# Performance work log

Hardware: AMD Instinct MI355X
Metric: run time of the kernel (lower is better)

## Reference

```python
import jax, jax.numpy as jnp
import numpy as np

N = 100_000      # nodes
E = 1_600_000    # edges
INP = 32
OUT = 32
ATTN = 32        # attn_rel_emb_dim
NREL = 16
NBASE = 8


def setup_inputs() -> dict:
    key = jax.random.key(0)
    ks = jax.random.split(key, 12)
    s = 0.1
    h = jax.random.normal(ks[0], (N, INP), jnp.float32)
    src = jax.random.randint(ks[1], (E,), 0, N)
    dst = jax.random.randint(ks[2], (E,), 0, N)
    e_type = jax.random.randint(ks[3], (E,), 0, NREL)
    weight = jax.random.normal(ks[4], (NBASE, INP, OUT), jnp.float32) * s
    w_comp = jax.random.normal(ks[5], (NREL, NBASE), jnp.float32) * s
    self_loop_weight = jax.random.normal(ks[6], (INP, OUT), jnp.float32) * s
    bias = jax.random.normal(ks[7], (OUT,), jnp.float32) * s
    attn_emb = jax.random.normal(ks[8], (NREL, ATTN), jnp.float32) * s
    A_w = jax.random.normal(ks[9], (2 * INP + ATTN, ATTN), jnp.float32) * s
    A_b = jnp.zeros((ATTN,), jnp.float32)
    B_w = jax.random.normal(ks[10], (ATTN, 1), jnp.float32) * s
    B_b = jnp.zeros((1,), jnp.float32)
    return dict(h=h, weight=weight, w_comp=w_comp, self_loop_weight=self_loop_weight,
                bias=bias, attn_emb=attn_emb, A_w=A_w, A_b=A_b, B_w=B_w, B_b=B_b,
                src=src, dst=dst, e_type=e_type)


def reference(h, weight, w_comp, self_loop_weight, bias, attn_emb,
              A_w, A_b, B_w, B_b, src, dst, e_type):
    # basis-decomposed relation weights: [num_rels, inp, out]
    rel_w = jnp.einsum('rb,bio->rio', w_comp, weight)
    # in-degree based scale (torch.log(in_degrees + 1); scale /= scale.mean())
    in_deg = jax.ops.segment_sum(jnp.ones((E,), h.dtype), dst, num_segments=N)
    scale = jnp.log(in_deg + 1.0)
    scale = scale / jnp.mean(scale)
    # per-edge message: gather relation weight, bmm with source feature
    msg = jnp.einsum('ei,eio->eo', h[src], rel_w[e_type])          # [E, OUT]
    # attention MLP over [h_src, h_dst, rel_emb]
    feat = jnp.concatenate([h[src], h[dst], attn_emb[e_type]], axis=1)  # [E, 2*INP+ATTN]
    a = jax.nn.sigmoid(jax.nn.relu(feat @ A_w + A_b) @ B_w + B_b)  # [E, 1]
    # scatter-reduce attended messages into destination nodes
    agg = jax.ops.segment_sum(a * msg, dst, num_segments=N)        # [N, OUT]
    # self-loop term (curr_emb in the aggregator)
    curr = h @ self_loop_weight                                     # [N, OUT]
    denom = jnp.maximum(in_deg, 1.0)[:, None]  # nei_edge_count normalization
    out = curr + scale[:, None] * agg / denom + bias
    return jax.nn.relu(out)
```

## Files before the change

kernel.cpp:

```cpp
#include <hip/hip_runtime.h>
#include <hip/hip_fp16.h>
#include <cstdio>
#include <cstdint>

#define NREL 16
#define NBASE 8
#define NPB 512
#define NPLACE 256

typedef _Float16 half8 __attribute__((ext_vector_type(8)));
typedef float floatx4 __attribute__((ext_vector_type(4)));

template <int CTRL>
__device__ __forceinline__ float dpp_add_f(float x) {
    int xi = __builtin_bit_cast(int, x);
    int yi = __builtin_amdgcn_update_dpp(0, xi, CTRL, 0xF, 0xF, true);
    return x + __builtin_bit_cast(float, yi);
}

__global__ __launch_bounds__(256) void k_fused1(
        const float* __restrict__ h, const float* __restrict__ A_w,
        const float* __restrict__ slw,
        const float* __restrict__ weight, const float* __restrict__ w_comp,
        const float* __restrict__ attn_emb, const float* __restrict__ A_b,
        const int* __restrict__ dst,
        __half* __restrict__ hA1, _Float16* __restrict__ h16,
        float* __restrict__ hA2, float* __restrict__ curr,
        _Float16* __restrict__ relwB16, float* __restrict__ relA,
        int* __restrict__ histT,
        int N, int E, int nb_pre) {
    __shared__ __align__(16) float Wall[32 * 128];
    __shared__ float hbuf[32 * 33];
    __shared__ int hist[256];
    int bx = blockIdx.x;
    int t = threadIdx.x;
    if (bx < nb_pre) {
        #pragma unroll
        for (int k = 0; k < 16; ++k) {
            int idx = t + 256 * k;
            int i = idx >> 7, c = idx & 127;
            float v = 0.f;
            if (c < 32)       v = A_w[i * 32 + c];
            else if (c < 64)  v = A_w[(32 + i) * 32 + (c - 32)];
            else if (c < 96)  v = slw[i * 32 + (c - 64)];
            Wall[idx] = v;
        }
        int n0 = bx * 32;
        #pragma unroll
        for (int k = 0; k < 4; ++k) {
            int idx = t + 256 * k;
            int row = idx >> 5, col = idx & 31;
            int n = n0 + row;
            hbuf[row * 33 + col] = (n < N) ? h[n * 32 + col] : 0.f;
        }
        __syncthreads();
        int nl = t >> 3;
        int tg = t & 7;
        float4 a0 = {0,0,0,0}, a1 = {0,0,0,0}, a2 = {0,0,0,0};
        #pragma unroll 8
        for (int i = 0; i < 32; ++i) {
            float hv = hbuf[nl * 33 + i];
            float4 w0 = *(const float4*)&Wall[i * 128 + tg * 12];
            float4 w1 = *(const float4*)&Wall[i * 128 + tg * 12 + 4];
            float4 w2 = *(const float4*)&Wall[i * 128 + tg * 12 + 8];
            a0.x += hv * w0.x; a0.y += hv * w0.y; a0.z += hv * w0.z; a0.w += hv * w0.w;
            a1.x += hv * w1.x; a1.y += hv * w1.y; a1.z += hv * w1.z; a1.w += hv * w1.w;
            a2.x += hv * w2.x; a2.y += hv * w2.y; a2.z += hv * w2.z; a2.w += hv * w2.w;
        }
        int n = n0 + nl;
        if (n < N) {
            float4 acc[3] = {a0, a1, a2};
            #pragma unroll
            for (int j = 0; j < 3; ++j) {
                int c = tg * 12 + j * 4;
                if (c < 32) {
                    *(__half2*)&hA1[n * 32 + c]     = __floats2half2_rn(acc[j].x, acc[j].y);
                    *(__half2*)&hA1[n * 32 + c + 2] = __floats2half2_rn(acc[j].z, acc[j].w);
                    __half2 p0 = __floats2half2_rn(hbuf[nl * 33 + c], hbuf[nl * 33 + c + 1]);
                    __half2 p1 = __floats2half2_rn(hbuf[nl * 33 + c + 2], hbuf[nl * 33 + c + 3]);
                    *(__half2*)&h16[n * 32 + c]     = p0;
                    *(__half2*)&h16[n * 32 + c + 2] = p1;
                } else if (c < 64) {
                    *(float4*)&hA2[n * 32 + (c - 32)] = acc[j];
                } else {
                    *(float4*)&curr[n * 32 + (c - 64)] = acc[j];
                }
            }
        }
    } else if (bx < nb_pre + 64) {
        int pidx = (bx - nb_pre) * 256 + t;
        int r = pidx >> 10, rem = pidx & 1023;
        int nb = rem >> 9, lj = rem & 511;
        int l = lj >> 3, j = lj & 7;
        int i = ((l >> 4) << 3) + j;
        int o = nb * 16 + (l & 15);
        float acc = 0.f;
        #pragma unroll
        for (int b = 0; b < NBASE; ++b)
            acc += w_comp[r * NBASE + b] * weight[b * 1024 + i * 32 + o];
        relwB16[pidx] = (_Float16)acc;
        if (pidx < 512) {
            int rr = pidx >> 5, oo = pidx & 31;
            float a = A_b[oo];
            #pragma unroll 8
            for (int ii = 0; ii < 32; ++ii)
                a += attn_emb[rr * 32 + ii] * A_w[(64 + ii) * 32 + oo];
            relA[pidx] = a;
        }
    } else {
        int nsb = (N + NPB - 1) / NPB;
        hist[t] = 0;
        __syncthreads();
        int blk = bx - (nb_pre + 64);
        int bpb = (E + NPLACE - 1) / NPLACE;
        int e0 = blk * bpb;
        int e1 = e0 + bpb; if (e1 > E) e1 = E;
        for (int e = e0 + t; e < e1; e += 256)
            atomicAdd(&hist[dst[e] >> 9], 1);
        __syncthreads();
        if (t < nsb) histT[t * NPLACE + blk] = hist[t];
    }
}

__global__ __launch_bounds__(NPLACE) void k_scanH(int* __restrict__ histT,
        int* __restrict__ binTot) {
    __shared__ int sd[NPLACE];
    int bin = blockIdx.x, t = threadIdx.x;
    int v = histT[bin * NPLACE + t];
    sd[t] = v;
    __syncthreads();
    for (int off = 1; off < NPLACE; off <<= 1) {
        int x = (t >= off) ? sd[t - off] : 0;
        __syncthreads();
        sd[t] += x;
        __syncthreads();
    }
    histT[bin * NPLACE + t] = sd[t] - v;
    if (t == NPLACE - 1) binTot[bin] = sd[NPLACE - 1];
}

__global__ __launch_bounds__(1024) void k_scanB(int* __restrict__ binTot, int nsb) {
    __shared__ int sd[1024];
    __shared__ int carry;
    int t = threadIdx.x;
    if (t == 0) carry = 0;
    __syncthreads();
    for (int base = 0; base < nsb; base += 1024) {
        int v = (base + t < nsb) ? binTot[base + t] : 0;
        sd[t] = v;
        __syncthreads();
        for (int off = 1; off < 1024; off <<= 1) {
            int x = (t >= off) ? sd[t - off] : 0;
            __syncthreads();
            sd[t] += x;
            __syncthreads();
        }
        int c = carry;
        if (base + t < nsb) binTot[base + t] = sd[t] - v + c;
        int tot = sd[1023];
        __syncthreads();
        if (t == 0) carry = c + tot;
        __syncthreads();
    }
    if (t == 0) binTot[nsb] = carry;
}

__global__ __launch_bounds__(256) void k_fused2(
        const _Float16* __restrict__ h16, const _Float16* __restrict__ relwB16,
        __half* __restrict__ hrel16,
        const int* __restrict__ src, const int* __restrict__ dst,
        const int* __restrict__ et,
        const int* __restrict__ histT, const int* __restrict__ binTot,
        int* __restrict__ tmp,
        int N, int E, int nb_hrel) {
    __shared__ __align__(16) _Float16 tile[16 * 512];
    __shared__ int cur[256];
    int bx = blockIdx.x;
    int t = threadIdx.x;
    if (bx < nb_hrel) {
        int n0 = bx * 16;
        int l = t & 63, w = t >> 6;
        int ar = n0 + (l & 15);
        if (ar >= N) ar = N - 1;
        half8 af = *(const half8*)(h16 + (size_t)ar * 32 + ((l >> 4) << 3));
        #pragma unroll
        for (int gg = 0; gg < 8; ++gg) {
            int g = w * 8 + gg;
            half8 bf = *(const half8*)(relwB16 + (size_t)g * 512 + l * 8);
            floatx4 d = {0.f, 0.f, 0.f, 0.f};
            d = __builtin_amdgcn_mfma_f32_16x16x32_f16(af, bf, d, 0, 0, 0);
            #pragma unroll
            for (int q = 0; q < 4; ++q) {
                int row = ((l >> 4) << 2) + q;
                tile[row * 512 + g * 16 + (l & 15)] = (_Float16)d[q];
            }
        }
        __syncthreads();
        #pragma unroll
        for (int p = 0; p < 4; ++p) {
            int idx = p * 256 + t;
            int row = idx >> 6, c8 = (idx & 63) << 3;
            int n = n0 + row;
            if (n < N)
                *(uint4*)&hrel16[(size_t)n * 512 + c8] = *(const uint4*)&tile[row * 512 + c8];
        }
    } else {
        int nsb = (N + NPB - 1) / NPB;
        int blk = bx - nb_hrel;
        if (t < nsb) cur[t] = histT[t * NPLACE + blk] + binTot[t];
        __syncthreads();
        int bpb = (E + NPLACE - 1) / NPLACE;
        int e0 = blk * bpb;
        int e1 = e0 + bpb; if (e1 > E) e1 = E;
        for (int e = e0 + t; e < e1; e += 256) {
            int d = dst[e];
            int pos = atomicAdd(&cur[d >> 9], 1);
            tmp[pos] = src[e] | (et[e] << 17) | ((d & 511) << 21);
        }
    }
}

__global__ __launch_bounds__(256) void k_sortbin(
        const int* __restrict__ tmp, int* __restrict__ packed,
        const int* __restrict__ binTot,
        int* __restrict__ rowptr, float* __restrict__ scale_s,
        int N, int E) {
    __shared__ int cnt[NPB];
    __shared__ int sa[256];
    __shared__ float sf[256];
    int t = threadIdx.x;
    int bin = blockIdx.x;
    int n0 = bin * NPB;
    cnt[t] = 0; cnt[t + 256] = 0;
    __syncthreads();
    int start = binTot[bin], end = binTot[bin + 1];
    for (int i = start + t; i < end; i += 256)
        atomicAdd(&cnt[(tmp[i] >> 21) & 511], 1);
    __syncthreads();
    int c0 = cnt[2 * t], c1 = cnt[2 * t + 1];
    sa[t] = c0 + c1;
    __syncthreads();
    for (int off = 1; off < 256; off <<= 1) {
        int x = (t >= off) ? sa[t - off] : 0;
        __syncthreads();
        sa[t] += x;
        __syncthreads();
    }
    int excl0 = sa[t] - (c0 + c1);
    int excl1 = excl0 + c0;
    int nA = n0 + 2 * t, nB = n0 + 2 * t + 1;
    if (nA <= N) rowptr[nA] = start + excl0;
    if (nB <= N) rowptr[nB] = start + excl1;
    float f = 0.f;
    if (nA < N) f += logf((float)c0 + 1.f);
    if (nB < N) f += logf((float)c1 + 1.f);
    sf[t] = f;
    __syncthreads();
    for (int s2 = 128; s2 > 0; s2 >>= 1) {
        if (t < s2) sf[t] += sf[t + s2];
        __syncthreads();
    }
    if (t == 0) atomicAdd(scale_s, sf[0]);
    cnt[2 * t] = start + excl0;
    cnt[2 * t + 1] = start + excl1;
    __syncthreads();
    for (int i = start + t; i < end; i += 256) {
        int rec = tmp[i];
        int dl = (rec >> 21) & 511;
        int pos = atomicAdd(&cnt[dl], 1);
        packed[pos] = rec;
    }
}

__global__ __launch_bounds__(256) void k_node_agg(
        const __half* __restrict__ hrel16, const __half* __restrict__ hA1,
        const float* __restrict__ hA2, const float* __restrict__ relA,
        const float* __restrict__ B_w, const float* __restrict__ B_b,
        const float* __restrict__ curr, const float* __restrict__ bias,
        const int* __restrict__ rowptr,
        const int* __restrict__ packed, const float* __restrict__ scale_s,
        float* __restrict__ out, int N) {
    int t = threadIdx.x;
    int wave = t >> 6, t64 = t & 63;
    int half = t64 >> 5, o = t64 & 31;
    int n = blockIdx.x * 4 + wave;
    if (n >= N) return;
    int r0 = rowptr[n], r1 = rowptr[n + 1];
    float hA2n = hA2[n * 32 + o];
    float bwo = B_w[o];
    float bb  = B_b[0];
    float acc = 0.f;
    for (int c0 = r0; c0 < r1; c0 += 64) {
        int j = c0 + t64;
        int pk = (j < r1) ? packed[j] : 0;
        int m = r1 - c0; if (m > 64) m = 64;
        for (int k = 0; k < m; k += 4) {
            int idxA = k + half;
            int idxB = k + 2 + half;
            int pkA = __shfl(pk, idxA, 64);
            int pkB = __shfl(pk, idxB, 64);
            int sA = pkA & 0x1FFFF, rA = (pkA >> 17) & 15;
            int sB = pkB & 0x1FFFF, rB = (pkB >> 17) & 15;
            float msgA = __half2float(hrel16[(size_t)sA * 512 + (rA << 5) + o]);
            float a1A  = __half2float(hA1[(sA << 5) + o]);
            float msgB = __half2float(hrel16[(size_t)sB * 512 + (rB << 5) + o]);
            float a1B  = __half2float(hA1[(sB << 5) + o]);
            float zA = a1A + hA2n + relA[(rA << 5) + o];
            float zB = a1B + hA2n + relA[(rB << 5) + o];
            float pA = fmaxf(zA, 0.f) * bwo;
            float pB = fmaxf(zB, 0.f) * bwo;
            pA = dpp_add_f<0x111>(pA); pB = dpp_add_f<0x111>(pB);
            pA = dpp_add_f<0x112>(pA); pB = dpp_add_f<0x112>(pB);
            pA = dpp_add_f<0x114>(pA); pB = dpp_add_f<0x114>(pB);
            pA = dpp_add_f<0x118>(pA); pB = dpp_add_f<0x118>(pB);
            pA = dpp_add_f<0x142>(pA); pB = dpp_add_f<0x142>(pB);
            pA = __shfl(pA, 31, 32) + bb;
            pB = __shfl(pB, 31, 32) + bb;
            float aA = 1.f / (1.f + __expf(-pA));
            float aB = 1.f / (1.f + __expf(-pB));
            acc += (idxA < m) ? aA * msgA : 0.f;
            acc += (idxB < m) ? aB * msgB : 0.f;
        }
    }
    acc += __shfl_xor(acc, 32, 64);
    if (half == 0) {
        float deg = (float)(r1 - r0);
        float smean = scale_s[0] / (float)N;
        float scale = logf(deg + 1.0f);
        float v = curr[n * 32 + o] + (scale / smean) * acc / fmaxf(deg, 1.f) + bias[o];
        out[n * 32 + o] = fmaxf(v, 0.f);
    }
}

extern "C" void kernel_launch(void* const* d_in, const int* in_sizes, int n_in,
                              void* d_out, int out_size, void* d_ws, size_t ws_size,
                              hipStream_t stream) {
    const float* h        = (const float*)d_in[0];
    const float* weight   = (const float*)d_in[1];
    const float* w_comp   = (const float*)d_in[2];
    const float* slw      = (const float*)d_in[3];
    const float* bias     = (const float*)d_in[4];
    const float* attn_emb = (const float*)d_in[5];
    const float* A_w      = (const float*)d_in[6];
    const float* A_b      = (const float*)d_in[7];
    const float* B_w      = (const float*)d_in[8];
    const float* B_b      = (const float*)d_in[9];
    const int*   src      = (const int*)d_in[10];
    const int*   dst      = (const int*)d_in[11];
    const int*   et       = (const int*)d_in[12];
    float*       out      = (float*)d_out;

    int N = in_sizes[0] / 32;
    int E = in_sizes[10];
    int nsb = (N + NPB - 1) / NPB;

    char* ws = (char*)d_ws;
    size_t off = 0;
    auto alloc = [&](size_t nbytes) {
        char* p = ws + off;
        off += (nbytes + 63) & ~((size_t)63);
        return p;
    };
    float*     scale_s = (float*)    alloc(4);
    size_t zero_bytes = off;
    int*       rowptr  = (int*)      alloc((size_t)(N + 1) * 4);
    int*       histT   = (int*)      alloc((size_t)nsb * NPLACE * 4);
    int*       binTot  = (int*)      alloc((size_t)(nsb + 1) * 4);
    _Float16*  relwB16 = (_Float16*) alloc((size_t)NREL * 1024 * 2);
    float*     relA    = (float*)    alloc((size_t)NREL * 32 * 4);
    __half*    hA1     = (__half*)   alloc((size_t)N * 32 * 2);
    _Float16*  h16     = (_Float16*) alloc((size_t)N * 32 * 2);
    float*     hA2     = (float*)    alloc((size_t)N * 32 * 4);
    float*     curr    = (float*)    alloc((size_t)N * 32 * 4);
    int*       tmp     = (int*)      alloc((size_t)E * 4);
    int*       packed  = (int*)      alloc((size_t)E * 4);
    __half*    hrel16  = (__half*)   alloc((size_t)N * 512 * 2);
    size_t need = off;

    if (ws_size < need) {
        fprintf(stderr, "kernel_launch: ws too small (%zu < %zu bytes) — no work launched\n",
                ws_size, need);
        return;
    }

    (void)hipMemsetAsync(d_ws, 0, zero_bytes, stream);

    int nb_pre = (N + 31) / 32;
    k_fused1<<<nb_pre + 64 + NPLACE, 256, 0, stream>>>(
        h, A_w, slw, weight, w_comp, attn_emb, A_b, dst,
        hA1, h16, hA2, curr, relwB16, relA, histT, N, E, nb_pre);

    k_scanH<<<nsb, NPLACE, 0, stream>>>(histT, binTot);
    k_scanB<<<1, 1024, 0, stream>>>(binTot, nsb);

    int nb_hrel = (N + 15) / 16;
    k_fused2<<<nb_hrel + NPLACE, 256, 0, stream>>>(
        h16, relwB16, hrel16, src, dst, et, histT, binTot, tmp, N, E, nb_hrel);

    k_sortbin<<<nsb, 256, 0, stream>>>(tmp, packed, binTot, rowptr, scale_s, N, E);

    k_node_agg<<<(N + 3) / 4, 256, 0, stream>>>(
        hrel16, hA1, hA2, relA, B_w, B_b, curr, bias,
        rowptr, packed, scale_s, out, N);
}
```

Before: 175.5 us.

## Use MFMA for node projections, move relation prep into scan kernel, unroll aggregation

```diff
diff --git a/kernel.cpp b/kernel.cpp
--- a/kernel.cpp
+++ b/kernel.cpp
@@ -21,74 +21,95 @@
 __global__ __launch_bounds__(256) void k_fused1(
         const float* __restrict__ h, const float* __restrict__ A_w,
         const float* __restrict__ slw,
-        const float* __restrict__ weight, const float* __restrict__ w_comp,
-        const float* __restrict__ attn_emb, const float* __restrict__ A_b,
         const int* __restrict__ dst,
         __half* __restrict__ hA1, _Float16* __restrict__ h16,
         float* __restrict__ hA2, float* __restrict__ curr,
-        _Float16* __restrict__ relwB16, float* __restrict__ relA,
         int* __restrict__ histT,
         int N, int E, int nb_pre) {
-    __shared__ __align__(16) float Wall[32 * 128];
-    __shared__ float hbuf[32 * 33];
     __shared__ int hist[256];
     int bx = blockIdx.x;
     int t = threadIdx.x;
     if (bx < nb_pre) {
+        int w = t >> 6, l = t & 63;
+        int n0 = bx * 64 + w * 16;
+        if (n0 >= N) return;
+        int lr = l & 15, lg = l >> 4;
+        int anode = n0 + lr;
+        int arc = (anode < N) ? anode : N - 1;
+        int ac = lg * 8;
+        float4 hv0 = *(const float4*)&h[(size_t)arc * 32 + ac];
+        float4 hv1 = *(const float4*)&h[(size_t)arc * 32 + ac + 4];
+        half8 af;
+        af[0] = (_Float16)hv0.x; af[1] = (_Float16)hv0.y;
+        af[2] = (_Float16)hv0.z; af[3] = (_Float16)hv0.w;
+        af[4] = (_Float16)hv1.x; af[5] = (_Float16)hv1.y;
+        af[6] = (_Float16)hv1.z; af[7] = (_Float16)hv1.w;
+        if (anode < N)
+            *(uint4*)&h16[(size_t)anode * 32 + ac] = *(const uint4*)&af;
         #pragma unroll
-        for (int k = 0; k < 16; ++k) {
-            int idx = t + 256 * k;
-            int i = idx >> 7, c = idx & 127;
-            float v = 0.f;
-            if (c < 32)       v = A_w[i * 32 + c];
-            else if (c < 64)  v = A_w[(32 + i) * 32 + (c - 32)];
-            else if (c < 96)  v = slw[i * 32 + (c - 64)];
-            Wall[idx] = v;
-        }
-        int n0 = bx * 32;
-        #pragma unroll
-        for (int k = 0; k < 4; ++k) {
-            int idx = t + 256 * k;
-            int row = idx >> 5, col = idx & 31;
-            int n = n0 + row;
-            hbuf[row * 33 + col] = (n < N) ? h[n * 32 + col] : 0.f;
-        }
-        __syncthreads();
-        int nl = t >> 3;
-        int tg = t & 7;
-        float4 a0 = {0,0,0,0}, a1 = {0,0,0,0}, a2 = {0,0,0,0};
-        #pragma unroll 8
-        for (int i = 0; i < 32; ++i) {
-            float hv = hbuf[nl * 33 + i];
-            float4 w0 = *(const float4*)&Wall[i * 128 + tg * 12];
-            float4 w1 = *(const float4*)&Wall[i * 128 + tg * 12 + 4];
-            float4 w2 = *(const float4*)&Wall[i * 128 + tg * 12 + 8];
-            a0.x += hv * w0.x; a0.y += hv * w0.y; a0.z += hv * w0.z; a0.w += hv * w0.w;
-            a1.x += hv * w1.x; a1.y += hv * w1.y; a1.z += hv * w1.z; a1.w += hv * w1.w;
-            a2.x += hv * w2.x; a2.y += hv * w2.y; a2.z += hv * w2.z; a2.w += hv * w2.w;
-        }
-        int n = n0 + nl;
-        if (n < N) {
-            float4 acc[3] = {a0, a1, a2};
+        for (int g = 0; g < 6; ++g) {
+            half8 bf;
             #pragma unroll
-            for (int j = 0; j < 3; ++j) {
-                int c = tg * 12 + j * 4;
-                if (c < 32) {
-                    *(__half2*)&hA1[n * 32 + c]     = __floats2half2_rn(acc[j].x, acc[j].y);
-                    *(__half2*)&hA1[n * 32 + c + 2] = __floats2half2_rn(acc[j].z, acc[j].w);
-                    __half2 p0 = __floats2half2_rn(hbuf[nl * 33 + c], hbuf[nl * 33 + c + 1]);
-                    __half2 p1 = __floats2half2_rn(hbuf[nl * 33 + c + 2], hbuf[nl * 33 + c + 3]);
-                    *(__half2*)&h16[n * 32 + c]     = p0;
-                    *(__half2*)&h16[n * 32 + c + 2] = p1;
-                } else if (c < 64) {
-                    *(float4*)&hA2[n * 32 + (c - 32)] = acc[j];
-                } else {
-                    *(float4*)&curr[n * 32 + (c - 64)] = acc[j];
+            for (int j = 0; j < 8; ++j) {
+                int i = lg * 8 + j;
+                int oc = g * 16 + lr;
+                float v;
+                if (g < 2)      v = A_w[i * 32 + oc];
+                else if (g < 4) v = A_w[(32 + i) * 32 + (oc - 32)];
+                else            v = slw[i * 32 + (oc - 64)];
+                bf[j] = (_Float16)v;
+            }
+            floatx4 d = {0.f, 0.f, 0.f, 0.f};
+            d = __builtin_amdgcn_mfma_f32_16x16x32_f16(af, bf, d, 0, 0, 0);
+            #pragma unroll
+            for (int q = 0; q < 4; ++q) {
+                int node = n0 + lg * 4 + q;
+                int oc = g * 16 + lr;
+                if (node < N) {
+                    if (g < 2)      hA1[(size_t)node * 32 + oc] = __float2half(d[q]);
+                    else if (g < 4) hA2[(size_t)node * 32 + (oc - 32)] = d[q];
+                    else            curr[(size_t)node * 32 + (oc - 64)] = d[q];
                 }
             }
         }
-    } else if (bx < nb_pre + 64) {
-        int pidx = (bx - nb_pre) * 256 + t;
+    } else {
+        int nsb = (N + NPB - 1) / NPB;
+        hist[t] = 0;
+        __syncthreads();
+        int blk = bx - nb_pre;
+        int bpb = (E + NPLACE - 1) / NPLACE;
+        int e0 = blk * bpb;
+        int e1 = e0 + bpb; if (e1 > E) e1 = E;
+        for (int e = e0 + t; e < e1; e += 256)
+            atomicAdd(&hist[dst[e] >> 9], 1);
+        __syncthreads();
+        if (t < nsb) histT[t * NPLACE + blk] = hist[t];
+    }
+}
+
+__global__ __launch_bounds__(NPLACE) void k_scanH_prep(
+        int* __restrict__ histT, int* __restrict__ binTot,
+        const float* __restrict__ weight, const float* __restrict__ w_comp,
+        const float* __restrict__ attn_emb, const float* __restrict__ A_w,
+        const float* __restrict__ A_b,
+        _Float16* __restrict__ relwB16, float* __restrict__ relA, int nsb) {
+    __shared__ int sd[NPLACE];
+    int bx = blockIdx.x, t = threadIdx.x;
+    if (bx < nsb) {
+        int bin = bx;
+        int v = histT[bin * NPLACE + t];
+        sd[t] = v;
+        __syncthreads();
+        for (int off = 1; off < NPLACE; off <<= 1) {
+            int x = (t >= off) ? sd[t - off] : 0;
+            __syncthreads();
+            sd[t] += x;
+            __syncthreads();
+        }
+        histT[bin * NPLACE + t] = sd[t] - v;
+        if (t == NPLACE - 1) binTot[bin] = sd[NPLACE - 1];
+    } else {
+        int pidx = (bx - nsb) * 256 + t;
         int r = pidx >> 10, rem = pidx & 1023;
         int nb = rem >> 9, lj = rem & 511;
         int l = lj >> 3, j = lj & 7;
@@ -107,36 +128,7 @@
                 a += attn_emb[rr * 32 + ii] * A_w[(64 + ii) * 32 + oo];
             relA[pidx] = a;
         }
-    } else {
-        int nsb = (N + NPB - 1) / NPB;
-        hist[t] = 0;
-        __syncthreads();
-        int blk = bx - (nb_pre + 64);
-        int bpb = (E + NPLACE - 1) / NPLACE;
-        int e0 = blk * bpb;
-        int e1 = e0 + bpb; if (e1 > E) e1 = E;
-        for (int e = e0 + t; e < e1; e += 256)
-            atomicAdd(&hist[dst[e] >> 9], 1);
-        __syncthreads();
-        if (t < nsb) histT[t * NPLACE + blk] = hist[t];
-    }
-}
-
-__global__ __launch_bounds__(NPLACE) void k_scanH(int* __restrict__ histT,
-        int* __restrict__ binTot) {
-    __shared__ int sd[NPLACE];
-    int bin = blockIdx.x, t = threadIdx.x;
-    int v = histT[bin * NPLACE + t];
-    sd[t] = v;
-    __syncthreads();
-    for (int off = 1; off < NPLACE; off <<= 1) {
-        int x = (t >= off) ? sd[t - off] : 0;
-        __syncthreads();
-        sd[t] += x;
-        __syncthreads();
-    }
-    histT[bin * NPLACE + t] = sd[t] - v;
-    if (t == NPLACE - 1) binTot[bin] = sd[NPLACE - 1];
+    }
 }
 
 __global__ __launch_bounds__(1024) void k_scanB(int* __restrict__ binTot, int nsb) {
@@ -280,7 +272,11 @@
         const int* __restrict__ rowptr,
         const int* __restrict__ packed, const float* __restrict__ scale_s,
         float* __restrict__ out, int N) {
+    __shared__ float relA_l[512];
     int t = threadIdx.x;
+    relA_l[t] = relA[t];
+    relA_l[t + 256] = relA[t + 256];
+    __syncthreads();
     int wave = t >> 6, t64 = t & 63;
     int half = t64 >> 5, o = t64 & 31;
     int n = blockIdx.x * 4 + wave;
@@ -294,32 +290,54 @@
         int j = c0 + t64;
         int pk = (j < r1) ? packed[j] : 0;
         int m = r1 - c0; if (m > 64) m = 64;
-        for (int k = 0; k < m; k += 4) {
-            int idxA = k + half;
-            int idxB = k + 2 + half;
-            int pkA = __shfl(pk, idxA, 64);
-            int pkB = __shfl(pk, idxB, 64);
+        for (int k = 0; k < m; k += 8) {
+            int iA = k + half, iB = k + 2 + half, iC = k + 4 + half, iD = k + 6 + half;
+            int pkA = __shfl(pk, iA, 64);
+            int pkB = __shfl(pk, iB, 64);
+            int pkC = __shfl(pk, iC, 64);
+            int pkD = __shfl(pk, iD, 64);
             int sA = pkA & 0x1FFFF, rA = (pkA >> 17) & 15;
             int sB = pkB & 0x1FFFF, rB = (pkB >> 17) & 15;
+            int sC = pkC & 0x1FFFF, rC = (pkC >> 17) & 15;
+            int sD = pkD & 0x1FFFF, rD = (pkD >> 17) & 15;
             float msgA = __half2float(hrel16[(size_t)sA * 512 + (rA << 5) + o]);
+            float msgB = __half2float(hrel16[(size_t)sB * 512 + (rB << 5) + o]);
+            float msgC = __half2float(hrel16[(size_t)sC * 512 + (rC << 5) + o]);
+            float msgD = __half2float(hrel16[(size_t)sD * 512 + (rD << 5) + o]);
             float a1A  = __half2float(hA1[(sA << 5) + o]);
-            float msgB = __half2float(hrel16[(size_t)sB * 512 + (rB << 5) + o]);
             float a1B  = __half2float(hA1[(sB << 5) + o]);
-            float zA = a1A + hA2n + relA[(rA << 5) + o];
-            float zB = a1B + hA2n + relA[(rB << 5) + o];
+            float a1C  = __half2float(hA1[(sC << 5) + o]);
+            float a1D  = __half2float(hA1[(sD << 5) + o]);
+            float zA = a1A + hA2n + relA_l[(rA << 5) + o];
+            float zB = a1B + hA2n + relA_l[(rB << 5) + o];
+            float zC = a1C + hA2n + relA_l[(rC << 5) + o];
+            float zD = a1D + hA2n + relA_l[(rD << 5) + o];
             float pA = fmaxf(zA, 0.f) * bwo;
             float pB = fmaxf(zB, 0.f) * bwo;
+            float pC = fmaxf(zC, 0.f) * bwo;
+            float pD = fmaxf(zD, 0.f) * bwo;
             pA = dpp_add_f<0x111>(pA); pB = dpp_add_f<0x111>(pB);
+            pC = dpp_add_f<0x111>(pC); pD = dpp_add_f<0x111>(pD);
             pA = dpp_add_f<0x112>(pA); pB = dpp_add_f<0x112>(pB);
+            pC = dpp_add_f<0x112>(pC); pD = dpp_add_f<0x112>(pD);
             pA = dpp_add_f<0x114>(pA); pB = dpp_add_f<0x114>(pB);
+            pC = dpp_add_f<0x114>(pC); pD = dpp_add_f<0x114>(pD);
             pA = dpp_add_f<0x118>(pA); pB = dpp_add_f<0x118>(pB);
+            pC = dpp_add_f<0x118>(pC); pD = dpp_add_f<0x118>(pD);
             pA = dpp_add_f<0x142>(pA); pB = dpp_add_f<0x142>(pB);
+            pC = dpp_add_f<0x142>(pC); pD = dpp_add_f<0x142>(pD);
             pA = __shfl(pA, 31, 32) + bb;
             pB = __shfl(pB, 31, 32) + bb;
+            pC = __shfl(pC, 31, 32) + bb;
+            pD = __shfl(pD, 31, 32) + bb;
             float aA = 1.f / (1.f + __expf(-pA));
             float aB = 1.f / (1.f + __expf(-pB));
-            acc += (idxA < m) ? aA * msgA : 0.f;
-            acc += (idxB < m) ? aB * msgB : 0.f;
+            float aC = 1.f / (1.f + __expf(-pC));
+            float aD = 1.f / (1.f + __expf(-pD));
+            acc += (iA < m) ? aA * msgA : 0.f;
+            acc += (iB < m) ? aB * msgB : 0.f;
+            acc += (iC < m) ? aC * msgC : 0.f;
+            acc += (iD < m) ? aD * msgD : 0.f;
         }
     }
     acc += __shfl_xor(acc, 32, 64);
@@ -385,12 +403,12 @@
 
     (void)hipMemsetAsync(d_ws, 0, zero_bytes, stream);
 
-    int nb_pre = (N + 31) / 32;
-    k_fused1<<<nb_pre + 64 + NPLACE, 256, 0, stream>>>(
-        h, A_w, slw, weight, w_comp, attn_emb, A_b, dst,
-        hA1, h16, hA2, curr, relwB16, relA, histT, N, E, nb_pre);
-
-    k_scanH<<<nsb, NPLACE, 0, stream>>>(histT, binTot);
+    int nb_pre = (N + 63) / 64;
+    k_fused1<<<nb_pre + NPLACE, 256, 0, stream>>>(
+        h, A_w, slw, dst, hA1, h16, hA2, curr, histT, N, E, nb_pre);
+
+    k_scanH_prep<<<nsb + 64, NPLACE, 0, stream>>>(
+        histT, binTot, weight, w_comp, attn_emb, A_w, A_b, relwB16, relA, nsb);
     k_scanB<<<1, 1024, 0, stream>>>(binTot, nsb);
 
     int nb_hrel = (N + 15) / 16;
```

After: 163.1 us. -7.1%, faster.
